# Kernel optimization log

Hardware: AMD Instinct MI355X
Metric: run time of the kernel (lower is better)

Reference implementation:

```python
import math
import jax, jax.numpy as jnp
import numpy as np

T_STEPS = 65536
T_S = 1.0      # net_params['t_s']
THETA = 10.0   # net_params['af_params']['theta']


def _eps_func(mult, tau, epsilon, t_end, t_s):
    vals = []
    for t in np.arange(0, t_end, t_s):
        v = mult * t / tau * math.exp(1 - t / tau)
        if abs(v) < abs(epsilon) and t > tau:
            break
        vals.append(v)
    return vals


def _srm_kernel(mult, tau, epsilon, t_end, t_s):
    # replicates SlayerTrainer._calculate_srm_kernel: pad-to-odd, prepend zeros, flip
    k = _eps_func(mult, tau, epsilon, t_end, t_s)
    if len(k) % 2 == 0:
        k.append(0.0)
    k = np.asarray(k, dtype=np.float32)
    k = np.concatenate([np.zeros(len(k) - 1, np.float32), k])[::-1].copy()
    return k  # (K,), K odd; causal after cross-correlation with pad K//2


def setup_inputs() -> dict:
    key = jax.random.key(0)
    k1, k2, k3 = jax.random.split(key, 3)
    x = jax.random.uniform(k1, (1, 1, 1, 250, T_STEPS), jnp.float32)
    srm = jnp.asarray(_srm_kernel(1.0, 10.0, 1e-4, 200, T_S))                 # sr_params
    ref = jnp.asarray(np.asarray(_eps_func(-20.0, 1.0, 1e-4, 200, T_S), np.float32))  # ref_params
    # SpikeLinear weights, init N(0, std=weights_init)
    w1 = jax.random.normal(k2, (25, 250), jnp.float32) * 4.0
    w2 = jax.random.normal(k3, (1, 25), jnp.float32) * 4.0
    return {"x": x, "srm": srm, "ref": ref, "w1": w1, "w2": w2}


def srm_conv(z, srm):
    # z: (C, T). Per-channel 1-D cross-correlation with 'same' padding,
    # equal to F.conv3d(x, eye-SRM kernel, padding=(0,0,K//2)) * t_s.
    K = srm.shape[0]
    p = K // 2
    lhs = z[:, None, :]            # (C, 1, T) -- channels as batch
    rhs = srm[None, None, :]       # (1, 1, K)
    out = jax.lax.conv_general_dilated(
        lhs, rhs, window_strides=(1,), padding=[(p, p)],
        dimension_numbers=("NCW", "OIW", "NCW"))
    return out[:, 0, :] * T_S


def gen_spikes(pot, ref):
    # Sequential integrate-fire with refractory feedback (slayer_cuda.get_spikes_cuda).
    # pot: (C, T). Carry = per-neuron buffer of scheduled future refractory additions.
    C = pot.shape[0]
    L = ref.shape[0]
    # ref[j] is added to potentials[t+j] on a spike at t (ref[0]==0); after the
    # shift, buf[0] corresponds to time t+1, so schedule ref[1:].
    ref_next = jnp.concatenate([ref[1:], jnp.zeros((1,), pot.dtype)])

    def step(buf, p_t):
        u = p_t + buf[:, 0]                           # membrane incl. refractory
        s = (u >= THETA).astype(pot.dtype)
        buf = jnp.concatenate([buf[:, 1:], jnp.zeros((C, 1), pot.dtype)], axis=1)
        buf = buf + s[:, None] * ref_next[None, :]
        return buf, (u, s / T_S)

    buf0 = jnp.zeros((C, L), pot.dtype)
    _, (u_seq, s_seq) = jax.lax.scan(step, buf0, pot.T)
    return u_seq.T, s_seq.T  # (C, T), (C, T)


def reference(x, srm, ref, w1, w2):
    h = srm_conv(x[0, 0, 0], srm)        # (250, T) SRM-filtered input spikes
    h = w1 @ h                           # (25, T)  SpikeLinear fc1
    _, s1 = gen_spikes(h, ref)           # (25, T)  spikes layer 1
    h = srm_conv(s1, srm)                # (25, T)  SRM on hidden spikes
    h = w2 @ h                           # (1, T)   SpikeLinear fc2
    _, s2 = gen_spikes(h, ref)           # (1, T)
    return s2.reshape(1, 1, 1, 1, -1)
```

## Files before the change

### kernel.cpp

```cpp
#include <hip/hip_runtime.h>


#define T_LEN   65536
#define NCH     250
#define NO1     25
#define KTAPS   129
#define PAD     128
#define SRM_LEN 257
#define REF_LEN 16
#define THETA_F 10.0f
#define LBLK    128
#define NBK     512
#define WARM    128
#define TS      256
#define TT      256
#define FTILE   1024
#define NWORDS  (T_LEN / 32)

__device__ __forceinline__ void srm_step(float p, const float (&rn)[15], float (&b)[15],
                                         unsigned &m, float &sf_out) {
  float u = p + b[0];
  unsigned sp = (u >= THETA_F) ? 1u : 0u;
  float sf = sp ? 1.0f : 0.0f;
#pragma unroll
  for (int j = 0; j < 14; ++j) b[j] = __builtin_fmaf(sf, rn[j], b[j + 1]);
  b[14] = __fmul_rn(sf, rn[14]);
  m = (m << 1) | sp;
  sf_out = sf;
}

__global__ void k_fill(float* out, float v) {
  out[blockIdx.x * 256 + threadIdx.x] = v;
}

__global__ __launch_bounds__(256) void k_prep(const float* __restrict__ w1,
                                              float* __restrict__ w1T) {
  for (int i = threadIdx.x; i < NO1 * NCH; i += 256) {
    int c = i / NO1, o = i - c * NO1;
    w1T[i] = w1[o * NCH + c];
  }
}

__global__ __launch_bounds__(256) void k_mm1(const float* __restrict__ x,
                                             const float* __restrict__ w1T,
                                             float* __restrict__ y1t) {
  __shared__ __align__(16) float wlds[NCH * NO1];
  __shared__ __align__(16) float part[4][13][TT];
  const int tid = threadIdx.x;
  const int lane = tid & 63;
  const int w = tid >> 6;
  const int t0 = blockIdx.x * TT;
  for (int j = tid * 4; j < NCH * NO1; j += 1024) {
    if (j + 4 <= NCH * NO1) *(float4*)&wlds[j] = *(const float4*)&w1T[j];
    else { for (int u = j; u < NCH * NO1; ++u) wlds[u] = w1T[u]; }
  }
  __syncthreads();
  const int cs = w * 62 + (w < 2 ? w : 2);
  const int cn = (w < 2) ? 63 : 62;
  const float* xp = x + (size_t)cs * T_LEN + t0 + lane * 4;
  float acc[NO1][4];
#pragma unroll
  for (int o = 0; o < NO1; ++o) { acc[o][0] = 0.f; acc[o][1] = 0.f; acc[o][2] = 0.f; acc[o][3] = 0.f; }
  float4 xb0 = *(const float4*)xp;
  float4 xb1 = *(const float4*)(xp + T_LEN);
  for (int ci = 0; ci < cn; ++ci) {
    float4 xv = xb0;
    xb0 = xb1;
    xb1 = (ci + 2 < cn) ? *(const float4*)(xp + (size_t)(ci + 2) * T_LEN)
                        : make_float4(0.f, 0.f, 0.f, 0.f);
    const float* wr = &wlds[(cs + ci) * NO1];
#pragma unroll
    for (int o = 0; o < NO1; ++o) {
      float wv = wr[o];
      acc[o][0] = __builtin_fmaf(wv, xv.x, acc[o][0]);
      acc[o][1] = __builtin_fmaf(wv, xv.y, acc[o][1]);
      acc[o][2] = __builtin_fmaf(wv, xv.z, acc[o][2]);
      acc[o][3] = __builtin_fmaf(wv, xv.w, acc[o][3]);
    }
  }
  float* yb = y1t + (size_t)blockIdx.x * (NO1 * TT);
#pragma unroll
  for (int r = 0; r < 2; ++r) {
    const int ob = r * 13;
    const int oc = r ? 12 : 13;
#pragma unroll
    for (int o = 0; o < 13; ++o) {
      if (o < oc)
        *(float4*)&part[w][o][lane * 4] =
            make_float4(acc[ob + o][0], acc[ob + o][1], acc[ob + o][2], acc[ob + o][3]);
    }
    __syncthreads();
    for (int j = tid; j < oc * (TT / 4); j += 256) {
      int o = j >> 6;
      int p4 = (j & 63) * 4;
      float4 a = *(const float4*)&part[0][o][p4];
      float4 b = *(const float4*)&part[1][o][p4];
      float4 c = *(const float4*)&part[2][o][p4];
      float4 d = *(const float4*)&part[3][o][p4];
      float4 rr;
      rr.x = __fadd_rn(__fadd_rn(__fadd_rn(a.x, b.x), c.x), d.x);
      rr.y = __fadd_rn(__fadd_rn(__fadd_rn(a.y, b.y), c.y), d.y);
      rr.z = __fadd_rn(__fadd_rn(__fadd_rn(a.z, b.z), c.z), d.z);
      rr.w = __fadd_rn(__fadd_rn(__fadd_rn(a.w, b.w), c.w), d.w);
      *(float4*)&yb[(ob + o) * TT + p4] = rr;
    }
    __syncthreads();
  }
}

__global__ __launch_bounds__(256, 8) void k_fir1(const float* __restrict__ y1t,
                                                 const float* __restrict__ srm,
                                                 float* __restrict__ pot1) {
  __shared__ __align__(16) float win[FTILE + PAD];
  const int tid = threadIdx.x;
  const int o = blockIdx.y;
  const int t0 = blockIdx.x * FTILE;
  for (int j = tid; j < FTILE + PAD; j += 256) {
    int g = t0 - PAD + j;
    win[j] = (g >= 0) ? y1t[(size_t)(g >> 8) * (NO1 * TT) + o * TT + (g & 255)] : 0.0f;
  }
  __syncthreads();
  const int base = tid * 4;
  float q0 = 0.0f, q1 = 0.0f, q2 = 0.0f, q3 = 0.0f;
#pragma unroll
  for (int i = 32; i >= 0; --i) {
    float4 v = *(const float4*)&win[base + 4 * i];
#pragma unroll
    for (int l = 3; l >= 0; --l) {
      float vl = (l == 0) ? v.x : (l == 1) ? v.y : (l == 2) ? v.z : v.w;
#pragma unroll
      for (int k = 0; k < 4; ++k) {
        int d = 128 + k - 4 * i - l;
        if (d >= 0 && d <= 128) {
          float e = srm[4 * i + l - k];
          if (k == 0) q0 = __builtin_fmaf(e, vl, q0);
          else if (k == 1) q1 = __builtin_fmaf(e, vl, q1);
          else if (k == 2) q2 = __builtin_fmaf(e, vl, q2);
          else q3 = __builtin_fmaf(e, vl, q3);
        }
      }
    }
  }
  *(float4*)&pot1[(size_t)o * T_LEN + t0 + base] = make_float4(q0, q1, q2, q3);
}

__global__ __launch_bounds__(TS) void k_pot2(const unsigned* __restrict__ s1p,
                                             const float* __restrict__ srm,
                                             const float* __restrict__ w2,
                                             float* __restrict__ pot2) {
  __shared__ float zs[TS + PAD];
  const int tid = threadIdx.x;
  const int t0 = blockIdx.x * TS;
  const int g0 = t0 - PAD;
  {
    int g = g0 + tid;
    float z = 0.0f;
    if (g >= 0) {
      int wi = g >> 5, sh = g & 31;
#pragma unroll
      for (int o = 0; o < NO1; ++o) {
        unsigned wv = s1p[o * NWORDS + wi];
        z += ((wv >> sh) & 1u) ? w2[o] : 0.0f;
      }
    }
    zs[tid] = z;
    if (tid < PAD) {
      int g2 = g0 + TS + tid;
      int wi = g2 >> 5, sh = g2 & 31;
      float z2 = 0.0f;
#pragma unroll
      for (int o = 0; o < NO1; ++o) {
        unsigned wv = s1p[o * NWORDS + wi];
        z2 += ((wv >> sh) & 1u) ? w2[o] : 0.0f;
      }
      zs[TS + tid] = z2;
    }
  }
  __syncthreads();
  float a = 0.0f;
#pragma unroll
  for (int d = 0; d < KTAPS; ++d) {
    float e = srm[PAD - d];
    a = __builtin_fmaf(e, zs[PAD + tid - d], a);
  }
  pot2[t0 + tid] = a;
}

template <int C, bool PACKED>
__global__ __launch_bounds__(64) void k_scan_spec(const float* __restrict__ pot,
                                                  const float* __restrict__ refk,
                                                  float* __restrict__ s,
                                                  unsigned* __restrict__ sp_,
                                                  unsigned* __restrict__ specin_m,
                                                  unsigned* __restrict__ specout_m,
                                                  float* __restrict__ specout_b) {
  int idx = blockIdx.x * 64 + threadIdx.x;
  if (idx >= C * NBK) return;
  int c = idx / NBK;
  int bb = idx - c * NBK;
  int tsr = bb * LBLK - WARM;
  float rn[15];
#pragma unroll
  for (int j = 0; j < 15; ++j) rn[j] = refk[j + 1];
  float b[15];
#pragma unroll
  for (int j = 0; j < 15; ++j) b[j] = 0.0f;
  unsigned m = 0;
  const float* prow = pot + (size_t)c * T_LEN;
  float* srow = PACKED ? nullptr : (s + (size_t)c * T_LEN);
  unsigned* srowp = PACKED ? (sp_ + (size_t)c * NWORDS) : nullptr;
  for (int k = 0; k < WARM + LBLK; k += 4) {
    if (k == WARM) specin_m[idx] = m & 0x7FFFu;
    int t = tsr + k;
    if (t < 0) continue;
    float4 pv = *(const float4*)(prow + t);
    float s0, s1v, s2, s3;
    srm_step(pv.x, rn, b, m, s0);
    srm_step(pv.y, rn, b, m, s1v);
    srm_step(pv.z, rn, b, m, s2);
    srm_step(pv.w, rn, b, m, s3);
    if (k >= WARM) {
      if (PACKED) {
        if (((t + 3) & 31) == 31) srowp[(t - 28) >> 5] = __brev(m);
      } else {
        *(float4*)(srow + t) = make_float4(s0, s1v, s2, s3);
      }
    }
  }
  specout_m[idx] = m & 0x7FFFu;
#pragma unroll
  for (int j = 0; j < 15; ++j) specout_b[idx * 16 + j] = b[j];
}

template <int C, bool PACKED>
__global__ __launch_bounds__(64) void k_scan_fix(const float* __restrict__ pot,
                                                 const float* __restrict__ refk,
                                                 float* __restrict__ s,
                                                 unsigned* __restrict__ sp_,
                                                 const unsigned* __restrict__ specin_m,
                                                 const unsigned* __restrict__ specout_m,
                                                 const float* __restrict__ specout_b) {
  const int c = blockIdx.x;
  const int lane = threadIdx.x;
  float rn[15];
#pragma unroll
  for (int j = 0; j < 15; ++j) rn[j] = refk[j + 1];
  float b[15];
#pragma unroll
  for (int j = 0; j < 15; ++j) b[j] = 0.0f;
  unsigned m = 0;
  bool haveB = true;
  const float* prow = pot + (size_t)c * T_LEN;
  float* srow = PACKED ? nullptr : (s + (size_t)c * T_LEN);
  unsigned* srowp = PACKED ? (sp_ + (size_t)c * NWORDS) : nullptr;
  unsigned prev_last = 0;

  unsigned siv[NBK / 64], sov[NBK / 64];
#pragma unroll
  for (int g = 0; g < NBK / 64; ++g) {
    siv[g] = specin_m[c * NBK + g * 64 + lane];
    sov[g] = specout_m[c * NBK + g * 64 + lane];
  }
#pragma unroll
  for (int g = 0; g < NBK / 64; ++g) {
    const unsigned si = siv[g];
    const unsigned so = sov[g];
    unsigned so_prev = __shfl_up(so, 1);
    if (lane == 0) so_prev = prev_last;
    const unsigned long long flags = __ballot(si == so_prev);
    prev_last = __shfl(so, 63);
    const unsigned si0 = __shfl(si, 0);
    if (flags == ~0ull && (m & 0x7FFFu) == si0) {
      m = prev_last;
      haveB = false;
      continue;
    }
    for (int r = 0; r < 64; ++r) {
      const unsigned sir = __shfl(si, r);
      const unsigned sor = __shfl(so, r);
      if ((m & 0x7FFFu) == sir) {
        m = sor;
        haveB = false;
      } else {
        const int bbr = g * 64 + r;
        if (!haveB) {
          const int pb = (c * NBK + bbr - 1) * 16;
#pragma unroll
          for (int q2 = 0; q2 < 15; ++q2) b[q2] = specout_b[pb + q2];
          haveB = true;
        }
        const int t0 = bbr * LBLK;
        for (int t = t0; t < t0 + LBLK; t += 4) {
          float4 pv = *(const float4*)(prow + t);
          float s0, s1v, s2, s3;
          srm_step(pv.x, rn, b, m, s0);
          srm_step(pv.y, rn, b, m, s1v);
          srm_step(pv.z, rn, b, m, s2);
          srm_step(pv.w, rn, b, m, s3);
          if (PACKED) {
            if ((((t + 3) & 31) == 31) && lane == 0) srowp[(t - 28) >> 5] = __brev(m);
          } else {
            if (lane == 0) *(float4*)(srow + t) = make_float4(s0, s1v, s2, s3);
          }
        }
        haveB = true;
      }
    }
  }
}

extern "C" void kernel_launch(void* const* d_in, const int* in_sizes, int n_in,
                              void* d_out, int out_size, void* d_ws, size_t ws_size,
                              hipStream_t stream) {
  const float* x    = (const float*)d_in[0];
  const float* srm  = (const float*)d_in[1];
  const float* refk = (const float*)d_in[2];
  const float* w1   = (const float*)d_in[3];
  const float* w2   = (const float*)d_in[4];
  float* out = (float*)d_out;

  float bad = 0.0f;
  if (n_in != 5) bad = 3.0f;
  else if (in_sizes[0] != NCH * T_LEN) bad = 4.0f;
  else if (in_sizes[1] != SRM_LEN)     bad = 5.0f;
  else if (in_sizes[2] != REF_LEN)     bad = 6.0f;
  else if (in_sizes[3] != NO1 * NCH)   bad = 7.0f;
  else if (in_sizes[4] != NO1)         bad = 8.0f;
  else if (out_size != T_LEN)          bad = 9.0f;
  if (bad != 0.0f) {
    k_fill<<<T_LEN / 256, 256, 0, stream>>>(out, bad);
    return;
  }

  size_t off = 0;
  auto alloc = [&](size_t bytes) { size_t o = off; off = (off + bytes + 255) & ~(size_t)255; return o; };
  char* ws = (char*)d_ws;
  size_t oY1  = alloc((size_t)NO1 * T_LEN * 4);
  size_t oP1  = alloc((size_t)NO1 * T_LEN * 4);
  size_t oS1P = alloc((size_t)NO1 * NWORDS * 4);
  size_t oP2  = alloc((size_t)T_LEN * 4);
  size_t oW1T = alloc((size_t)NO1 * NCH * 4);
  if (ws_size < off) {
    k_fill<<<T_LEN / 256, 256, 0, stream>>>(out, 2.0f);
    return;
  }

  float*    y1t  = (float*)(ws + oY1);
  float*    pot1 = (float*)(ws + oP1);
  unsigned* s1p  = (unsigned*)(ws + oS1P);
  float*    pot2 = (float*)(ws + oP2);
  float*    w1T  = (float*)(ws + oW1T);
  char* yb = ws + oY1;
  unsigned* si1 = (unsigned*)(yb);
  unsigned* so1 = (unsigned*)(yb + 51200);
  float*    sb1 = (float*)   (yb + 102400);
  unsigned* si2 = (unsigned*)(yb + 921600);
  unsigned* so2 = (unsigned*)(yb + 923648);
  float*    sb2 = (float*)   (yb + 925696);

  k_prep<<<1, 256, 0, stream>>>(w1, w1T);
  k_mm1<<<T_LEN / TT, 256, 0, stream>>>(x, w1T, y1t);
  k_fir1<<<dim3(T_LEN / FTILE, NO1), 256, 0, stream>>>(y1t, srm, pot1);
  k_scan_spec<NO1, true><<<(NO1 * NBK + 63) / 64, 64, 0, stream>>>(
      pot1, refk, nullptr, s1p, si1, so1, sb1);
  k_scan_fix<NO1, true><<<NO1, 64, 0, stream>>>(pot1, refk, nullptr, s1p, si1, so1, sb1);
  k_pot2<<<T_LEN / TS, TS, 0, stream>>>(s1p, srm, w2, pot2);
  k_scan_spec<1, false><<<(NBK + 63) / 64, 64, 0, stream>>>(
      pot2, refk, out, nullptr, si2, so2, sb2);
  k_scan_fix<1, false><<<1, 64, 0, stream>>>(pot2, refk, out, nullptr, si2, so2, sb2);
}
```

Measured before the change: 99.68 us.

## Split mm1 channel reduction across 16 wavefronts and read weights as scalars

New measurement: 95.11 us. -4.6%, faster.

```diff
diff --git a/kernel.cpp b/kernel.cpp
--- a/kernel.cpp
+++ b/kernel.cpp
@@ -16,6 +16,7 @@
 #define TT      256
 #define FTILE   1024
 #define NWORDS  (T_LEN / 32)
+#define NGRP    16
 
 __device__ __forceinline__ void srm_step(float p, const float (&rn)[15], float (&b)[15],
                                          unsigned &m, float &sf_out) {
@@ -41,26 +42,23 @@
   }
 }
 
-__global__ __launch_bounds__(256) void k_mm1(const float* __restrict__ x,
-                                             const float* __restrict__ w1T,
-                                             float* __restrict__ y1t) {
-  __shared__ __align__(16) float wlds[NCH * NO1];
-  __shared__ __align__(16) float part[4][13][TT];
+__global__ __launch_bounds__(1024, 4) void k_mm1(const float* __restrict__ x,
+                                                 const float* __restrict__ w1T,
+                                                 float* __restrict__ y1t) {
+  __shared__ __align__(16) float part[NGRP][5][TT];
   const int tid = threadIdx.x;
   const int lane = tid & 63;
-  const int w = tid >> 6;
+  const int wv = __builtin_amdgcn_readfirstlane(tid >> 6);
   const int t0 = blockIdx.x * TT;
-  for (int j = tid * 4; j < NCH * NO1; j += 1024) {
-    if (j + 4 <= NCH * NO1) *(float4*)&wlds[j] = *(const float4*)&w1T[j];
-    else { for (int u = j; u < NCH * NO1; ++u) wlds[u] = w1T[u]; }
-  }
-  __syncthreads();
-  const int cs = w * 62 + (w < 2 ? w : 2);
-  const int cn = (w < 2) ? 63 : 62;
+  const int cs = wv * 15 + (wv < 10 ? wv : 10);
+  const int cn = (wv < 10) ? 16 : 15;
+  float acc[NO1][4];
+#pragma unroll
+  for (int o = 0; o < NO1; ++o) {
+    acc[o][0] = 0.f; acc[o][1] = 0.f; acc[o][2] = 0.f; acc[o][3] = 0.f;
+  }
   const float* xp = x + (size_t)cs * T_LEN + t0 + lane * 4;
-  float acc[NO1][4];
-#pragma unroll
-  for (int o = 0; o < NO1; ++o) { acc[o][0] = 0.f; acc[o][1] = 0.f; acc[o][2] = 0.f; acc[o][3] = 0.f; }
+  const float* wt = w1T + cs * NO1;
   float4 xb0 = *(const float4*)xp;
   float4 xb1 = *(const float4*)(xp + T_LEN);
   for (int ci = 0; ci < cn; ++ci) {
@@ -68,41 +66,39 @@
     xb0 = xb1;
     xb1 = (ci + 2 < cn) ? *(const float4*)(xp + (size_t)(ci + 2) * T_LEN)
                         : make_float4(0.f, 0.f, 0.f, 0.f);
-    const float* wr = &wlds[(cs + ci) * NO1];
+    const float* wr = wt + ci * NO1;
 #pragma unroll
     for (int o = 0; o < NO1; ++o) {
-      float wv = wr[o];
-      acc[o][0] = __builtin_fmaf(wv, xv.x, acc[o][0]);
-      acc[o][1] = __builtin_fmaf(wv, xv.y, acc[o][1]);
-      acc[o][2] = __builtin_fmaf(wv, xv.z, acc[o][2]);
-      acc[o][3] = __builtin_fmaf(wv, xv.w, acc[o][3]);
+      float wvv = wr[o];
+      acc[o][0] = __builtin_fmaf(wvv, xv.x, acc[o][0]);
+      acc[o][1] = __builtin_fmaf(wvv, xv.y, acc[o][1]);
+      acc[o][2] = __builtin_fmaf(wvv, xv.z, acc[o][2]);
+      acc[o][3] = __builtin_fmaf(wvv, xv.w, acc[o][3]);
     }
   }
   float* yb = y1t + (size_t)blockIdx.x * (NO1 * TT);
 #pragma unroll
-  for (int r = 0; r < 2; ++r) {
-    const int ob = r * 13;
-    const int oc = r ? 12 : 13;
-#pragma unroll
-    for (int o = 0; o < 13; ++o) {
-      if (o < oc)
-        *(float4*)&part[w][o][lane * 4] =
-            make_float4(acc[ob + o][0], acc[ob + o][1], acc[ob + o][2], acc[ob + o][3]);
+  for (int r = 0; r < 5; ++r) {
+#pragma unroll
+    for (int oo = 0; oo < 5; ++oo) {
+      int o = r * 5 + oo;
+      *(float4*)&part[wv][oo][lane * 4] =
+          make_float4(acc[o][0], acc[o][1], acc[o][2], acc[o][3]);
     }
     __syncthreads();
-    for (int j = tid; j < oc * (TT / 4); j += 256) {
-      int o = j >> 6;
-      int p4 = (j & 63) * 4;
-      float4 a = *(const float4*)&part[0][o][p4];
-      float4 b = *(const float4*)&part[1][o][p4];
-      float4 c = *(const float4*)&part[2][o][p4];
-      float4 d = *(const float4*)&part[3][o][p4];
-      float4 rr;
-      rr.x = __fadd_rn(__fadd_rn(__fadd_rn(a.x, b.x), c.x), d.x);
-      rr.y = __fadd_rn(__fadd_rn(__fadd_rn(a.y, b.y), c.y), d.y);
-      rr.z = __fadd_rn(__fadd_rn(__fadd_rn(a.z, b.z), c.z), d.z);
-      rr.w = __fadd_rn(__fadd_rn(__fadd_rn(a.w, b.w), c.w), d.w);
-      *(float4*)&yb[(ob + o) * TT + p4] = rr;
+    if (tid < 5 * (TT / 4)) {
+      int oo = tid >> 6;
+      int p4 = (tid & 63) * 4;
+      float4 s = *(const float4*)&part[0][oo][p4];
+#pragma unroll
+      for (int g = 1; g < NGRP; ++g) {
+        float4 p = *(const float4*)&part[g][oo][p4];
+        s.x = __fadd_rn(s.x, p.x);
+        s.y = __fadd_rn(s.y, p.y);
+        s.z = __fadd_rn(s.z, p.z);
+        s.w = __fadd_rn(s.w, p.w);
+      }
+      *(float4*)&yb[(r * 5 + oo) * TT + p4] = s;
     }
     __syncthreads();
   }
@@ -159,8 +155,8 @@
       int wi = g >> 5, sh = g & 31;
 #pragma unroll
       for (int o = 0; o < NO1; ++o) {
-        unsigned wv = s1p[o * NWORDS + wi];
-        z += ((wv >> sh) & 1u) ? w2[o] : 0.0f;
+        unsigned wvv = s1p[o * NWORDS + wi];
+        z += ((wvv >> sh) & 1u) ? w2[o] : 0.0f;
       }
     }
     zs[tid] = z;
@@ -170,8 +166,8 @@
       float z2 = 0.0f;
 #pragma unroll
       for (int o = 0; o < NO1; ++o) {
-        unsigned wv = s1p[o * NWORDS + wi];
-        z2 += ((wv >> sh) & 1u) ? w2[o] : 0.0f;
+        unsigned wvv = s1p[o * NWORDS + wi];
+        z2 += ((wvv >> sh) & 1u) ? w2[o] : 0.0f;
       }
       zs[TS + tid] = z2;
     }
@@ -359,7 +355,7 @@
   float*    sb2 = (float*)   (yb + 925696);
 
   k_prep<<<1, 256, 0, stream>>>(w1, w1T);
-  k_mm1<<<T_LEN / TT, 256, 0, stream>>>(x, w1T, y1t);
+  k_mm1<<<T_LEN / TT, 1024, 0, stream>>>(x, w1T, y1t);
   k_fir1<<<dim3(T_LEN / FTILE, NO1), 256, 0, stream>>>(y1t, srm, pot1);
   k_scan_spec<NO1, true><<<(NO1 * NBK + 63) / 64, 64, 0, stream>>>(
       pot1, refk, nullptr, s1p, si1, so1, sb1);
```
